# Kernel tuning notes

Measured on AMD Instinct MI355X. Metric: run time of the kernel, lower is better.

Reference implementation:

```python
import jax, jax.numpy as jnp
import numpy as np


def _extract_patches(img, px, py, sx, sy):
    # TF tf.image.extract_patches with 'SAME' padding; returns (b, oh, ow, px, py, C)
    b, h, w, C = img.shape
    oh, ow = -(-h // sx), -(-w // sy)
    ph = max((oh - 1) * sx + px - h, 0)
    pw = max((ow - 1) * sy + py - w, 0)
    pt, pl = ph // 2, pw // 2
    pad = jnp.pad(img, ((0, 0), (pt, ph - pt), (pl, pw - pl), (0, 0)))
    ri = np.arange(oh)[:, None] * sx + np.arange(px)[None, :]  # (oh, px)
    ci = np.arange(ow)[:, None] * sy + np.arange(py)[None, :]  # (ow, py)
    p = pad[:, ri][:, :, :, ci]  # (b, oh, px, ow, py, C)
    return jnp.transpose(p, (0, 1, 3, 2, 4, 5))


def _forward(mr_features, pet_features, b_features, px, py, sx, sy):
    b, h, w, c = pet_features.shape
    bb, bh, bw, bc, bf = b_features.shape
    lx, ly = px // sx, py // sy
    Nx, Ny = h // px, w // py
    SNx, SNy = Nx * lx, Ny * ly
    # im2col-style overlapping patch extraction
    bflat = b_features.reshape(bb, bh, bw, bc * bf)
    b_p = _extract_patches(bflat, px, py, sx, sy).reshape(bb, SNx, SNy, px, py, bc, bf)
    pet_p = _extract_patches(pet_features, px, py, sx, sy).reshape(b, SNx, SNy, px, py, bc, 1)
    # kernel-weighted per-patch normalization (divide_no_nan semantics)
    diag = jnp.sum(b_p, axis=(3, 4), keepdims=True)
    kp = jnp.sum(pet_p * b_p, axis=(3, 4), keepdims=True)
    safe = jnp.where(diag == 0, jnp.ones_like(diag), diag)
    kpn = jnp.where(diag == 0, jnp.zeros_like(kp), kp / safe) * b_p
    K = jnp.sum(kpn, axis=-1)  # (b, SNx, SNy, px, py, c)
    # de-interleave strided sub-grids: stk[k=j*lx+i] = K[:, i::lx, j::ly]
    K5 = K.reshape(b, Nx, lx, Ny, ly, px, py, c)
    stk = jnp.transpose(K5, (4, 2, 0, 1, 3, 5, 6, 7)).reshape(lx * ly, b, Nx, Ny, px, py, c)
    kp_ = jnp.transpose(stk, (1, 2, 3, 4, 5, 6, 0)).reshape(b, Nx, Ny, px, py, c, lx, ly)
    kp_ = jnp.transpose(kp_, (0, 1, 3, 2, 4, 5, 6, 7)).reshape(b, Nx * px, Ny * py, c, lx, ly)
    imgs = jnp.transpose(kp_, (4, 5, 0, 1, 2, 3))  # (lx, ly, b, H, W, c)
    # align_patches: roll-based realignment of the lx*ly shifted reconstructions
    H, W = Nx * px, Ny * py
    rollx = np.arange((-px) // 2 + sx // 2, px // 2 + sx // 2, sx)  # len lx
    rolly = np.arange((-py) // 2 + sy // 2, py // 2 + sy // 2, sy)  # len ly
    rev = jnp.transpose(imgs, (2, 3, 4, 5, 0, 1)).reshape(b, H, W, c, lx * ly)
    rev = jnp.transpose(rev, (4, 0, 1, 2, 3))  # (lx*ly, b, H, W, c)
    rolled = jnp.stack(
        [jnp.roll(rev[k], (int(rollx[k % lx]), int(rolly[k // lx])), axis=(1, 2))
         for k in range(lx * ly)], axis=0)
    return jnp.mean(rolled, axis=0)  # (b, H, W, c)


def setup_inputs() -> dict:
    key = jax.random.key(0)
    k1, k2, k3 = jax.random.split(key, 3)
    B, H, W, C, F = 2, 128, 128, 16, 16
    return {
        "mr_features": jax.random.normal(k1, (B, H, W, C), dtype=jnp.float32),
        "pet_features": jax.random.uniform(k2, (B, H, W, C), dtype=jnp.float32),
        "b_features": jax.random.uniform(k3, (B, H, W, C, F), dtype=jnp.float32),
        "px": 8, "py": 8, "sx": 4, "sy": 4,
    }


def reference(mr_features, pet_features, b_features, px, py, sx, sy):
    return _forward(mr_features, pet_features, b_features, px, py, sx, sy)
```

## Files before the change

kernel.cpp:

```cpp
#include <hip/hip_runtime.h>
#include <cstddef>

#define HH 128
#define WW 128
#define CC 16
#define FF 16

__global__ __launch_bounds__(256) void fused_kernel(
    const float*  __restrict__ pet,
    const float4* __restrict__ bfe4,
    float* __restrict__ out)
{
    __shared__ float4 sD[7 * 7 * 4];
    __shared__ float4 sK[7 * 7 * 4];
    __shared__ float4 sR[6 * 6 * 4];

    int bid = blockIdx.x;
    int tx = bid & 7;
    int ty = (bid >> 3) & 7;
    int ch = (bid >> 6) & 15;
    int b  = bid >> 10;

    int tid = threadIdx.x;
    int y0 = 16 * ty, x0 = 16 * tx;
    int gi0 = 4 * ty - 1, gj0 = 4 * tx - 1;

    if (tid < 196) {
        int f4 = tid & 3;
        int cc = tid >> 2;
        int cj = cc % 7, ci = cc / 7;
        int r0 = 4 * (gi0 + ci) - 2;
        int s0 = 4 * (gj0 + cj) - 2;
        float4 d = make_float4(0.f, 0.f, 0.f, 0.f);
        float4 k = make_float4(0.f, 0.f, 0.f, 0.f);
        #pragma unroll
        for (int p = 0; p < 4; ++p) {
            int r = r0 + p;
            if ((unsigned)r >= (unsigned)HH) continue;
            #pragma unroll
            for (int q = 0; q < 4; ++q) {
                int s = s0 + q;
                if ((unsigned)s >= (unsigned)WW) continue;
                int pix = (b * HH + r) * WW + s;
                float4 bv = bfe4[(size_t)pix * 64 + ch * 4 + f4];
                float  pv = pet[(size_t)pix * CC + ch];
                d.x += bv.x;      d.y += bv.y;      d.z += bv.z;      d.w += bv.w;
                k.x += pv * bv.x; k.y += pv * bv.y; k.z += pv * bv.z; k.w += pv * bv.w;
            }
        }
        sD[cc * 4 + f4] = d;
        sK[cc * 4 + f4] = k;
    }
    __syncthreads();

    if (tid < 144) {
        int f4 = tid & 3;
        int pc = tid >> 2;
        int pj = pc % 6, pi = pc / 6;
        float4 D = make_float4(0.f, 0.f, 0.f, 0.f);
        float4 K = make_float4(0.f, 0.f, 0.f, 0.f);
        #pragma unroll
        for (int di = 0; di < 2; ++di) {
            #pragma unroll
            for (int dj = 0; dj < 2; ++dj) {
                int cc = (pi + di) * 7 + (pj + dj);
                float4 cd = sD[cc * 4 + f4];
                float4 ck = sK[cc * 4 + f4];
                D.x += cd.x; D.y += cd.y; D.z += cd.z; D.w += cd.w;
                K.x += ck.x; K.y += ck.y; K.z += ck.z; K.w += ck.w;
            }
        }
        float4 rv;
        rv.x = (D.x != 0.f) ? K.x / D.x : 0.f;
        rv.y = (D.y != 0.f) ? K.y / D.y : 0.f;
        rv.z = (D.z != 0.f) ? K.z / D.z : 0.f;
        rv.w = (D.w != 0.f) ? K.w / D.w : 0.f;
        sR[pc * 4 + f4] = rv;
    }
    __syncthreads();

    int dy = tid >> 4, dx = tid & 15;
    int y = y0 + dy, x = x0 + dx;

    float rs[16];
    #pragma unroll
    for (int i = 0; i < 16; ++i) rs[i] = 0.f;

    #pragma unroll
    for (int il = 0; il < 2; ++il) {
        bool vy = il ? (y >= 2) : (y <= 125);
        int pi = il ? (2 * ((dy - 2) >> 3) + 2)
                    : (2 * ((dy + 2) >> 3) + 1);
        #pragma unroll
        for (int jl = 0; jl < 2; ++jl) {
            bool vx = jl ? (x >= 2) : (x <= 125);
            int pj = jl ? (2 * ((dx - 2) >> 3) + 2)
                        : (2 * ((dx + 2) >> 3) + 1);
            if (vy && vx) {
                int base = (pi * 6 + pj) * 4;
                #pragma unroll
                for (int v = 0; v < 4; ++v) {
                    float4 rv = sR[base + v];
                    rs[4*v+0] += rv.x; rs[4*v+1] += rv.y;
                    rs[4*v+2] += rv.z; rs[4*v+3] += rv.w;
                }
            }
        }
    }

    int pix = (b * HH + y) * WW + x;
    const float4* bp = bfe4 + (size_t)pix * 64 + ch * 4;
    float acc = 0.f;
    #pragma unroll
    for (int v = 0; v < 4; ++v) {
        float4 bv = bp[v];
        acc += rs[4*v+0] * bv.x + rs[4*v+1] * bv.y
             + rs[4*v+2] * bv.z + rs[4*v+3] * bv.w;
    }
    out[(size_t)pix * CC + ch] = 0.25f * acc;
}

extern "C" void kernel_launch(void* const* d_in, const int* in_sizes, int n_in,
                              void* d_out, int out_size, void* d_ws, size_t ws_size,
                              hipStream_t stream) {
    const float* pet = (const float*)d_in[1];
    const float* bfe = (const float*)d_in[2];
    int B = in_sizes[1] / (HH * WW * CC);

    int grid = B * 16 * 64;
    fused_kernel<<<grid, 256, 0, stream>>>(pet, (const float4*)bfe, (float*)d_out);
}
```

Measured before the change: 28.11 us.

## Precompute 4x4 cell sums in separate kernel to remove halo recomputation

Splits the fused kernel in two. The first kernel computes each 4x4 cell's D and K partial sums exactly once into workspace. The second kernel loads the 7x7 neighbourhood of cells from that workspace instead of re-reading b_features for overlapping halos in every tile. This removes the redundant halo reads and FMAs (each tile read 28x28 pixels to cover 16x16). The cost is an extra kernel launch and a global round trip for the cell arrays.

Result: faster. 24.77 us (-11.9%).

```diff
diff --git a/kernel.cpp b/kernel.cpp
--- a/kernel.cpp
+++ b/kernel.cpp
@@ -5,10 +5,52 @@
 #define WW 128
 #define CC 16
 #define FF 16
+#define NCELL 33
 
-__global__ __launch_bounds__(256) void fused_kernel(
-    const float*  __restrict__ pet,
+__global__ __launch_bounds__(256) void cell_kernel(
+    const float* __restrict__ pet,
     const float4* __restrict__ bfe4,
+    float4* __restrict__ cellD,
+    float4* __restrict__ cellK,
+    int total)
+{
+    int t = blockIdx.x * 256 + threadIdx.x;
+    if (t >= total) return;
+    int f4  = t & 3;
+    int ch  = (t >> 2) & 15;
+    int rest = t >> 6;
+    int j   = rest % NCELL;
+    int tmp = rest / NCELL;
+    int i   = tmp % NCELL;
+    int b   = tmp / NCELL;
+
+    int r0 = 4 * i - 2;
+    int s0 = 4 * j - 2;
+    float4 d = make_float4(0.f, 0.f, 0.f, 0.f);
+    float4 k = make_float4(0.f, 0.f, 0.f, 0.f);
+    #pragma unroll
+    for (int p = 0; p < 4; ++p) {
+        int r = r0 + p;
+        if ((unsigned)r >= (unsigned)HH) continue;
+        #pragma unroll
+        for (int q = 0; q < 4; ++q) {
+            int s = s0 + q;
+            if ((unsigned)s >= (unsigned)WW) continue;
+            int pix = (b * HH + r) * WW + s;
+            float4 bv = bfe4[(size_t)pix * 64 + ch * 4 + f4];
+            float  pv = pet[(size_t)pix * CC + ch];
+            d.x += bv.x;      d.y += bv.y;      d.z += bv.z;      d.w += bv.w;
+            k.x += pv * bv.x; k.y += pv * bv.y; k.z += pv * bv.z; k.w += pv * bv.w;
+        }
+    }
+    cellD[t] = d;
+    cellK[t] = k;
+}
+
+__global__ __launch_bounds__(256) void fused2_kernel(
+    const float4* __restrict__ bfe4,
+    const float4* __restrict__ cellD,
+    const float4* __restrict__ cellK,
     float* __restrict__ out)
 {
     __shared__ float4 sD[7 * 7 * 4];
@@ -23,33 +65,22 @@
 
     int tid = threadIdx.x;
     int y0 = 16 * ty, x0 = 16 * tx;
-    int gi0 = 4 * ty - 1, gj0 = 4 * tx - 1;
 
     if (tid < 196) {
         int f4 = tid & 3;
         int cc = tid >> 2;
         int cj = cc % 7, ci = cc / 7;
-        int r0 = 4 * (gi0 + ci) - 2;
-        int s0 = 4 * (gj0 + cj) - 2;
+        int gi = 4 * ty - 1 + ci;
+        int gj = 4 * tx - 1 + cj;
         float4 d = make_float4(0.f, 0.f, 0.f, 0.f);
         float4 k = make_float4(0.f, 0.f, 0.f, 0.f);
-        #pragma unroll
-        for (int p = 0; p < 4; ++p) {
-            int r = r0 + p;
-            if ((unsigned)r >= (unsigned)HH) continue;
-            #pragma unroll
-            for (int q = 0; q < 4; ++q) {
-                int s = s0 + q;
-                if ((unsigned)s >= (unsigned)WW) continue;
-                int pix = (b * HH + r) * WW + s;
-                float4 bv = bfe4[(size_t)pix * 64 + ch * 4 + f4];
-                float  pv = pet[(size_t)pix * CC + ch];
-                d.x += bv.x;      d.y += bv.y;      d.z += bv.z;      d.w += bv.w;
-                k.x += pv * bv.x; k.y += pv * bv.y; k.z += pv * bv.z; k.w += pv * bv.w;
-            }
+        if ((unsigned)gi < (unsigned)NCELL && (unsigned)gj < (unsigned)NCELL) {
+            size_t c = ((((size_t)b * NCELL + gi) * NCELL + gj) * CC + ch) * 4 + f4;
+            d = cellD[c];
+            k = cellK[c];
         }
-        sD[cc * 4 + f4] = d;
-        sK[cc * 4 + f4] = k;
+        sD[tid] = d;
+        sK[tid] = k;
     }
     __syncthreads();
 
@@ -127,6 +158,13 @@
     const float* bfe = (const float*)d_in[2];
     int B = in_sizes[1] / (HH * WW * CC);
 
+    int nCellVec = B * NCELL * NCELL * CC * FF / 4;
+    float4* cellD = (float4*)d_ws;
+    float4* cellK = cellD + nCellVec;
+
+    int gA = (nCellVec + 255) / 256;
+    cell_kernel<<<gA, 256, 0, stream>>>(pet, (const float4*)bfe, cellD, cellK, nCellVec);
+
     int grid = B * 16 * 64;
-    fused_kernel<<<grid, 256, 0, stream>>>(pet, (const float4*)bfe, (float*)d_out);
+    fused2_kernel<<<grid, 256, 0, stream>>>((const float4*)bfe, cellD, cellK, (float*)d_out);
 }
```

## Enlarge spatial tile to 32x32 per block to cut halo recomputation

Applied to the files above, without the earlier changes.

Each block now covers a 32x32 output tile per channel instead of 16x16. This shrinks the halo of 4x4 cell sums that must be recomputed, from 7x7 cells per 4x4 interior to 11x11 per 8x8, and lowers the number of global halo reads. Each thread now produces four output pixels. The grid drops from 2048 to 512 blocks, which may leave the GPU's compute units underused. A fast path also skips the bounds checks for interior cells.

After: 29.04 us. 3.3% more time.

```diff
diff --git a/kernel.cpp b/kernel.cpp
--- a/kernel.cpp
+++ b/kernel.cpp
@@ -4,66 +4,79 @@
 #define HH 128
 #define WW 128
 #define CC 16
-#define FF 16
 
-__global__ __launch_bounds__(256) void fused_kernel(
+__global__ __launch_bounds__(256) void fused32_kernel(
     const float*  __restrict__ pet,
     const float4* __restrict__ bfe4,
     float* __restrict__ out)
 {
-    __shared__ float4 sD[7 * 7 * 4];
-    __shared__ float4 sK[7 * 7 * 4];
-    __shared__ float4 sR[6 * 6 * 4];
+    __shared__ float4 sD[11 * 11 * 4];
+    __shared__ float4 sK[11 * 11 * 4];
+    __shared__ float4 sR[10 * 10 * 4];
 
     int bid = blockIdx.x;
-    int tx = bid & 7;
-    int ty = (bid >> 3) & 7;
-    int ch = (bid >> 6) & 15;
-    int b  = bid >> 10;
+    int tx = bid & 3;
+    int ty = (bid >> 2) & 3;
+    int ch = (bid >> 4) & 15;
+    int b  = bid >> 8;
 
     int tid = threadIdx.x;
-    int y0 = 16 * ty, x0 = 16 * tx;
-    int gi0 = 4 * ty - 1, gj0 = 4 * tx - 1;
+    int y0 = 32 * ty, x0 = 32 * tx;
+    int gi0 = 8 * ty - 1, gj0 = 8 * tx - 1;
 
-    if (tid < 196) {
-        int f4 = tid & 3;
-        int cc = tid >> 2;
-        int cj = cc % 7, ci = cc / 7;
+    for (int item = tid; item < 484; item += 256) {
+        int f4 = item & 3;
+        int cc = item >> 2;
+        int cj = cc % 11, ci = cc / 11;
         int r0 = 4 * (gi0 + ci) - 2;
         int s0 = 4 * (gj0 + cj) - 2;
         float4 d = make_float4(0.f, 0.f, 0.f, 0.f);
         float4 k = make_float4(0.f, 0.f, 0.f, 0.f);
-        #pragma unroll
-        for (int p = 0; p < 4; ++p) {
-            int r = r0 + p;
-            if ((unsigned)r >= (unsigned)HH) continue;
+        if (r0 >= 0 && r0 + 4 <= HH && s0 >= 0 && s0 + 4 <= WW) {
             #pragma unroll
-            for (int q = 0; q < 4; ++q) {
-                int s = s0 + q;
-                if ((unsigned)s >= (unsigned)WW) continue;
-                int pix = (b * HH + r) * WW + s;
-                float4 bv = bfe4[(size_t)pix * 64 + ch * 4 + f4];
-                float  pv = pet[(size_t)pix * CC + ch];
-                d.x += bv.x;      d.y += bv.y;      d.z += bv.z;      d.w += bv.w;
-                k.x += pv * bv.x; k.y += pv * bv.y; k.z += pv * bv.z; k.w += pv * bv.w;
+            for (int p = 0; p < 4; ++p) {
+                #pragma unroll
+                for (int q = 0; q < 4; ++q) {
+                    int pix = (b * HH + r0 + p) * WW + (s0 + q);
+                    float4 bv = bfe4[(size_t)pix * 64 + ch * 4 + f4];
+                    float  pv = pet[(size_t)pix * CC + ch];
+                    d.x += bv.x;      d.y += bv.y;      d.z += bv.z;      d.w += bv.w;
+                    k.x += pv * bv.x; k.y += pv * bv.y; k.z += pv * bv.z; k.w += pv * bv.w;
+                }
+            }
+        } else {
+            #pragma unroll
+            for (int p = 0; p < 4; ++p) {
+                int r = r0 + p;
+                if ((unsigned)r >= (unsigned)HH) continue;
+                #pragma unroll
+                for (int q = 0; q < 4; ++q) {
+                    int s = s0 + q;
+                    if ((unsigned)s >= (unsigned)WW) continue;
+                    int pix = (b * HH + r) * WW + s;
+                    float4 bv = bfe4[(size_t)pix * 64 + ch * 4 + f4];
+                    float  pv = pet[(size_t)pix * CC + ch];
+                    d.x += bv.x;      d.y += bv.y;      d.z += bv.z;      d.w += bv.w;
+                    k.x += pv * bv.x; k.y += pv * bv.y; k.z += pv * bv.z; k.w += pv * bv.w;
+                }
             }
         }
-        sD[cc * 4 + f4] = d;
-        sK[cc * 4 + f4] = k;
+        sD[item] = d;
+        sK[item] = k;
     }
     __syncthreads();
 
-    if (tid < 144) {
-        int f4 = tid & 3;
-        int pc = tid >> 2;
-        int pj = pc % 6, pi = pc / 6;
+    for (int item = tid; item < 400; item += 256) {
+        int f4 = item & 3;
+        int pc = item >> 2;
+        int pj = pc % 10, pi = pc / 10;
         float4 D = make_float4(0.f, 0.f, 0.f, 0.f);
         float4 K = make_float4(0.f, 0.f, 0.f, 0.f);
         #pragma unroll
         for (int di = 0; di < 2; ++di) {
             #pragma unroll
             for (int dj = 0; dj < 2; ++dj) {
-                int cc = (pi + di) * 7 + (pj + dj);
+                int cc = (pi + di) * 11 + (pj + dj);
                 float4 cd = sD[cc * 4 + f4];
                 float4 ck = sK[cc * 4 + f4];
                 D.x += cd.x; D.y += cd.y; D.z += cd.z; D.w += cd.w;
@@ -75,49 +88,53 @@
         rv.y = (D.y != 0.f) ? K.y / D.y : 0.f;
         rv.z = (D.z != 0.f) ? K.z / D.z : 0.f;
         rv.w = (D.w != 0.f) ? K.w / D.w : 0.f;
-        sR[pc * 4 + f4] = rv;
+        sR[item] = rv;
     }
     __syncthreads();
 
-    int dy = tid >> 4, dx = tid & 15;
-    int y = y0 + dy, x = x0 + dx;
+    #pragma unroll
+    for (int k3 = 0; k3 < 4; ++k3) {
+        int p  = tid + k3 * 256;
+        int dy = p >> 5, dx = p & 31;
+        int y = y0 + dy, x = x0 + dx;
 
-    float rs[16];
-    #pragma unroll
-    for (int i = 0; i < 16; ++i) rs[i] = 0.f;
+        float rs[16];
+        #pragma unroll
+        for (int i = 0; i < 16; ++i) rs[i] = 0.f;
 
-    #pragma unroll
-    for (int il = 0; il < 2; ++il) {
-        bool vy = il ? (y >= 2) : (y <= 125);
-        int pi = il ? (2 * ((dy - 2) >> 3) + 2)
-                    : (2 * ((dy + 2) >> 3) + 1);
         #pragma unroll
-        for (int jl = 0; jl < 2; ++jl) {
-            bool vx = jl ? (x >= 2) : (x <= 125);
-            int pj = jl ? (2 * ((dx - 2) >> 3) + 2)
-                        : (2 * ((dx + 2) >> 3) + 1);
-            if (vy && vx) {
-                int base = (pi * 6 + pj) * 4;
-                #pragma unroll
-                for (int v = 0; v < 4; ++v) {
-                    float4 rv = sR[base + v];
-                    rs[4*v+0] += rv.x; rs[4*v+1] += rv.y;
-                    rs[4*v+2] += rv.z; rs[4*v+3] += rv.w;
+        for (int il = 0; il < 2; ++il) {
+            bool vy = il ? (y >= 2) : (y <= 125);
+            int pi = il ? (2 * ((dy - 2) >> 3) + 2)
+                        : (2 * ((dy + 2) >> 3) + 1);
+            #pragma unroll
+            for (int jl = 0; jl < 2; ++jl) {
+                bool vx = jl ? (x >= 2) : (x <= 125);
+                int pj = jl ? (2 * ((dx - 2) >> 3) + 2)
+                            : (2 * ((dx + 2) >> 3) + 1);
+                if (vy && vx) {
+                    int base = (pi * 10 + pj) * 4;
+                    #pragma unroll
+                    for (int v = 0; v < 4; ++v) {
+                        float4 rv = sR[base + v];
+                        rs[4*v+0] += rv.x; rs[4*v+1] += rv.y;
+                        rs[4*v+2] += rv.z; rs[4*v+3] += rv.w;
+                    }
                 }
             }
         }
+
+        int pix = (b * HH + y) * WW + x;
+        const float4* bp = bfe4 + (size_t)pix * 64 + ch * 4;
+        float acc = 0.f;
+        #pragma unroll
+        for (int v = 0; v < 4; ++v) {
+            float4 bv = bp[v];
+            acc += rs[4*v+0] * bv.x + rs[4*v+1] * bv.y
+                 + rs[4*v+2] * bv.z + rs[4*v+3] * bv.w;
+        }
+        out[(size_t)pix * CC + ch] = 0.25f * acc;
     }
-
-    int pix = (b * HH + y) * WW + x;
-    const float4* bp = bfe4 + (size_t)pix * 64 + ch * 4;
-    float acc = 0.f;
-    #pragma unroll
-    for (int v = 0; v < 4; ++v) {
-        float4 bv = bp[v];
-        acc += rs[4*v+0] * bv.x + rs[4*v+1] * bv.y
-             + rs[4*v+2] * bv.z + rs[4*v+3] * bv.w;
-    }
-    out[(size_t)pix * CC + ch] = 0.25f * acc;
 }
 
 extern "C" void kernel_launch(void* const* d_in, const int* in_sizes, int n_in,
@@ -127,6 +144,6 @@
     const float* bfe = (const float*)d_in[2];
     int B = in_sizes[1] / (HH * WW * CC);
 
-    int grid = B * 16 * 64;
-    fused_kernel<<<grid, 256, 0, stream>>>(pet, (const float4*)bfe, (float*)d_out);
+    int grid = B * 16 * 16;
+    fused32_kernel<<<grid, 256, 0, stream>>>(pet, (const float4*)bfe, (float*)d_out);
 }
```
